# Performance work log

Measured on AMD Instinct MI355X. Metric: run time of the kernel, lower is better.

## Reference

```python
import jax, jax.numpy as jnp
import numpy as np

TEMPERATURE = 0.5
EPS = 1e-12  # torch F.normalize eps


def _l2_normalize(x, eps=EPS):
    n = jnp.linalg.norm(x, axis=1, keepdims=True)
    return x / jnp.maximum(n, eps)


def setup_inputs() -> dict:
    key = jax.random.key(0)
    k1, k2 = jax.random.split(key)
    B, D = 4096, 512
    return {
        "polyline_embs": jax.random.normal(k1, (B, D), dtype=jnp.float32),
        "c_embs": jax.random.normal(k2, (B, D), dtype=jnp.float32),
    }


def reference(polyline_embs, c_embs):
    b = polyline_embs.shape[0]
    # double-normalization in the original (F.normalize then cosine_similarity)
    # is idempotent on unit vectors, so sim = Z @ Z^T with Z unit-normalized.
    z = _l2_normalize(jnp.concatenate([polyline_embs, c_embs], axis=0))  # [2B, D]
    sim = z @ z.T  # [2B, 2B] cosine similarity
    # positives: diag offsets +B and -B
    idx = jnp.arange(b)
    sim_ij = sim[idx, idx + b]
    sim_ji = sim[idx + b, idx]
    positives = jnp.concatenate([sim_ij, sim_ji], axis=0)  # [2B]
    nominator = jnp.exp(positives / TEMPERATURE)
    mask = 1.0 - jnp.eye(2 * b, dtype=sim.dtype)
    denominator = jnp.sum(mask * jnp.exp(sim / TEMPERATURE), axis=1)  # [2B]
    all_losses = -jnp.log(nominator / denominator)
    return jnp.sum(all_losses) / (2 * b)
```

## Files before the change

kernel.cpp:

```cpp
#include <hip/hip_runtime.h>
#include <hip/hip_bf16.h>

#define B_ROWS 4096
#define D_DIM  512
#define N_ROWS 8192
#define BM 128
#define BN 128
#define BKB 128
#define NBLK (N_ROWS / BM)
#define NPAIR (NBLK * (NBLK + 1) / 2)

typedef float f32x4 __attribute__((ext_vector_type(4)));
typedef int   v4i   __attribute__((ext_vector_type(4)));
typedef int   v8i   __attribute__((ext_vector_type(8)));

__global__ __launch_bounds__(256) void prep_kernel(
    const float* __restrict__ poly, const float* __restrict__ cemb,
    unsigned char* __restrict__ Z, float* __restrict__ row_sum,
    float* __restrict__ pos, unsigned int* __restrict__ counter)
{
    const int wave = threadIdx.x >> 6;
    const int lane = threadIdx.x & 63;
    const int r = blockIdx.x * 4 + wave;

    const float4* prow = (const float4*)(poly + (size_t)r * D_DIM) + lane * 2;
    const float4* crow = (const float4*)(cemb + (size_t)r * D_DIM) + lane * 2;
    const float4 p0 = prow[0], p1 = prow[1];
    const float4 c0 = crow[0], c1 = crow[1];

    float ssp = p0.x*p0.x + p0.y*p0.y + p0.z*p0.z + p0.w*p0.w
              + p1.x*p1.x + p1.y*p1.y + p1.z*p1.z + p1.w*p1.w;
    float ssc = c0.x*c0.x + c0.y*c0.y + c0.z*c0.z + c0.w*c0.w
              + c1.x*c1.x + c1.y*c1.y + c1.z*c1.z + c1.w*c1.w;
    float dt  = p0.x*c0.x + p0.y*c0.y + p0.z*c0.z + p0.w*c0.w
              + p1.x*c1.x + p1.y*c1.y + p1.z*c1.z + p1.w*c1.w;

    #pragma unroll
    for (int m = 1; m < 64; m <<= 1) {
        ssp += __shfl_xor(ssp, m);
        ssc += __shfl_xor(ssc, m);
        dt  += __shfl_xor(dt,  m);
    }

    const float sp = 1.0f / fmaxf(sqrtf(ssp), 1e-12f);
    const float sc = 1.0f / fmaxf(sqrtf(ssc), 1e-12f);

    int2 zp, zc;
    zp.x = __builtin_amdgcn_cvt_pk_fp8_f32(p0.x*sp, p0.y*sp, 0, false)
         | (__builtin_amdgcn_cvt_pk_fp8_f32(p0.z*sp, p0.w*sp, 0, false) << 16);
    zp.y = __builtin_amdgcn_cvt_pk_fp8_f32(p1.x*sp, p1.y*sp, 0, false)
         | (__builtin_amdgcn_cvt_pk_fp8_f32(p1.z*sp, p1.w*sp, 0, false) << 16);
    zc.x = __builtin_amdgcn_cvt_pk_fp8_f32(c0.x*sc, c0.y*sc, 0, false)
         | (__builtin_amdgcn_cvt_pk_fp8_f32(c0.z*sc, c0.w*sc, 0, false) << 16);
    zc.y = __builtin_amdgcn_cvt_pk_fp8_f32(c1.x*sc, c1.y*sc, 0, false)
         | (__builtin_amdgcn_cvt_pk_fp8_f32(c1.z*sc, c1.w*sc, 0, false) << 16);

    *(int2*)(Z + (size_t)r * D_DIM + lane * 8)            = zp;
    *(int2*)(Z + (size_t)(r + B_ROWS) * D_DIM + lane * 8) = zc;

    if (lane == 0) {
        pos[r] = dt * sp * sc;
        row_sum[2 * r]     = 0.0f;
        row_sum[2 * r + 1] = 0.0f;
        if (r == 0) *counter = 0u;
    }
}

__global__ __launch_bounds__(512) void sim_kernel(
    const unsigned char* __restrict__ Z, float* __restrict__ row_sum,
    const float* __restrict__ pos, float* __restrict__ out,
    unsigned int* __restrict__ counter)
{
    __shared__ __align__(16) unsigned char As[BM * BKB];
    __shared__ __align__(16) unsigned char Bs[BN * BKB];
    __shared__ float rAcc[BM];
    __shared__ float cAcc[BN];
    __shared__ unsigned int lastFlag;

    const int t0 = blockIdx.x;
    int bi = (int)((129.0f - sqrtf(16641.0f - 8.0f * (float)t0)) * 0.5f);
    #define CFN(b) ((b) * (129 - (b)) / 2)
    while (CFN(bi + 1) <= t0) ++bi;
    while (CFN(bi) > t0) --bi;
    const int bj = bi + (t0 - CFN(bi));
    #undef CFN
    const bool diag = (bi == bj);

    const int ibase = bi * BM;
    const int jbase = bj * BN;
    const int tid   = threadIdx.x;

    const int srow = tid >> 3;
    const int gchk = (tid & 7) ^ (srow & 7);

    const int wave = tid >> 6;
    const int lane = tid & 63;
    const int wi = (wave >> 2) * 64;
    const int wj = (wave & 3) * 32;
    const int quad = lane >> 4;
    const int c    = lane & 15;

    f32x4 acc[4][2] = {};

    const int sg0 = (((quad << 1)    ) ^ (c & 7)) * 16;
    const int sg1 = (((quad << 1) | 1) ^ (c & 7)) * 16;

    #pragma unroll 1
    for (int k0 = 0; k0 < D_DIM; k0 += BKB) {
        #pragma unroll
        for (int it = 0; it < 2; ++it) {
            const int row = it * 64 + srow;
            const unsigned char* ga = Z + (size_t)(ibase + row) * D_DIM + k0 + gchk * 16;
            __builtin_amdgcn_global_load_lds(
                (const __attribute__((address_space(1))) void*)ga,
                (__attribute__((address_space(3))) void*)(As + it * 8192 + tid * 16),
                16, 0, 0);
        }
        if (!diag) {
            #pragma unroll
            for (int it = 0; it < 2; ++it) {
                const int row = it * 64 + srow;
                const unsigned char* gb = Z + (size_t)(jbase + row) * D_DIM + k0 + gchk * 16;
                __builtin_amdgcn_global_load_lds(
                    (const __attribute__((address_space(1))) void*)gb,
                    (__attribute__((address_space(3))) void*)(Bs + it * 8192 + tid * 16),
                    16, 0, 0);
            }
        }
        __syncthreads();

        const unsigned char* bb = diag ? As : Bs;

        v8i bfr[2];
        #pragma unroll
        for (int tj = 0; tj < 2; ++tj) {
            const unsigned char* base = bb + (wj + tj * 16 + c) * BKB;
            const v4i lo = *(const v4i*)(base + sg0);
            const v4i hi = *(const v4i*)(base + sg1);
            bfr[tj] = __builtin_shufflevector(lo, hi, 0, 1, 2, 3, 4, 5, 6, 7);
        }
        #pragma unroll
        for (int ti = 0; ti < 4; ++ti) {
            const unsigned char* base = As + (wi + ti * 16 + c) * BKB;
            const v4i lo = *(const v4i*)(base + sg0);
            const v4i hi = *(const v4i*)(base + sg1);
            const v8i afr = __builtin_shufflevector(lo, hi, 0, 1, 2, 3, 4, 5, 6, 7);
            #pragma unroll
            for (int tj = 0; tj < 2; ++tj)
                acc[ti][tj] = __builtin_amdgcn_mfma_scale_f32_16x16x128_f8f6f4(
                    afr, bfr[tj], acc[ti][tj],
                    0, 0,
                    0, 0x7f7f7f7f,
                    0, 0x7f7f7f7f);
        }
        __syncthreads();
    }

    if (tid < BM) { rAcc[tid] = 0.0f; cAcc[tid] = 0.0f; }
    __syncthreads();

    const float K2 = 2.885390081777927f;
    float col[2] = {0.0f, 0.0f};
    #pragma unroll
    for (int ti = 0; ti < 4; ++ti) {
        const int li = wi + ti * 16 + quad * 4;
        #pragma unroll
        for (int r = 0; r < 4; ++r) {
            const int gi = ibase + li + r;
            float v = 0.0f;
            #pragma unroll
            for (int tj = 0; tj < 2; ++tj) {
                const int gj = jbase + wj + tj * 16 + c;
                const float e = (gj > gi) ? exp2f(K2 * acc[ti][tj][r]) : 0.0f;
                v += e;
                col[tj] += e;
            }
            v += __shfl_xor(v, 1);
            v += __shfl_xor(v, 2);
            v += __shfl_xor(v, 4);
            v += __shfl_xor(v, 8);
            if (c == 0)
                atomicAdd(&rAcc[li + r], v);
        }
    }
    #pragma unroll
    for (int tj = 0; tj < 2; ++tj) {
        float w = col[tj];
        w += __shfl_xor(w, 16);
        w += __shfl_xor(w, 32);
        if (quad == 0)
            atomicAdd(&cAcc[wj + tj * 16 + c], w);
    }
    __syncthreads();

    if (tid < BM)
        atomicAdd(&row_sum[ibase + tid], rAcc[tid]);
    else if (tid < 2 * BM)
        atomicAdd(&row_sum[jbase + tid - BM], cAcc[tid - BM]);

    __syncthreads();
    if (tid == 0) {
        unsigned int old = __hip_atomic_fetch_add(
            counter, 1u, __ATOMIC_RELAXED, __HIP_MEMORY_SCOPE_AGENT);
        lastFlag = (old == NPAIR - 1) ? 1u : 0u;
    }
    __syncthreads();
    if (lastFlag) {
        float accL = 0.0f, accP = 0.0f;
        for (int i = tid; i < N_ROWS; i += 512) {
            const float rs = __hip_atomic_load(
                &row_sum[i], __ATOMIC_RELAXED, __HIP_MEMORY_SCOPE_AGENT);
            accL += __logf(rs);
        }
        for (int r = tid; r < B_ROWS; r += 512)
            accP += pos[r];
        #pragma unroll
        for (int m = 1; m < 64; m <<= 1) {
            accL += __shfl_xor(accL, m);
            accP += __shfl_xor(accP, m);
        }
        if (lane == 0) { rAcc[wave] = accL; cAcc[wave] = accP; }
        __syncthreads();
        if (tid == 0) {
            float L = 0.0f, P = 0.0f;
            #pragma unroll
            for (int w = 0; w < 8; ++w) { L += rAcc[w]; P += cAcc[w]; }
            out[0] = (L - 4.0f * P) / (float)N_ROWS;
        }
    }
}

extern "C" void kernel_launch(void* const* d_in, const int* in_sizes, int n_in,
                              void* d_out, int out_size, void* d_ws, size_t ws_size,
                              hipStream_t stream) {
    const float* poly = (const float*)d_in[0];
    const float* cemb = (const float*)d_in[1];

    unsigned char* Z       = (unsigned char*)d_ws;
    float*         row_sum = (float*)((char*)d_ws + (size_t)N_ROWS * D_DIM);
    float*         pos     = row_sum + N_ROWS;
    unsigned int*  counter = (unsigned int*)(pos + B_ROWS);
    float*         out     = (float*)d_out;

    prep_kernel<<<B_ROWS / 4, 256, 0, stream>>>(poly, cemb, Z, row_sum, pos, counter);
    sim_kernel<<<NPAIR, 512, 0, stream>>>(Z, row_sum, pos, out, counter);
}
```

Measured before the change: 121.0 us.

## Double-buffer LDS tiles and use DPP for intra-quad row reductions

Splits the LDS A/B tiles into two buffers so the async global-to-LDS load of the next K chunk is issued while MFMAs run on the current chunk, hiding load latency across the four K steps. It also swaps the first two shuffle-xor reduction steps for DPP quad-permute moves, which avoids LDS-based permutes. Doubling LDS to 64KB per block may lower occupancy. The loop keeps a single barrier per iteration, which raises the question of whether the next stage's writes can race with reads of the buffer still being consumed.

```diff
diff --git a/kernel.cpp b/kernel.cpp
--- a/kernel.cpp
+++ b/kernel.cpp
@@ -13,6 +13,15 @@
 typedef float f32x4 __attribute__((ext_vector_type(4)));
 typedef int   v4i   __attribute__((ext_vector_type(4)));
 typedef int   v8i   __attribute__((ext_vector_type(8)));
+
+__device__ __forceinline__ float dpp_xor1_add(float v) {
+    return v + __int_as_float(__builtin_amdgcn_mov_dpp(
+        __float_as_int(v), 0xB1, 0xf, 0xf, true));
+}
+__device__ __forceinline__ float dpp_xor2_add(float v) {
+    return v + __int_as_float(__builtin_amdgcn_mov_dpp(
+        __float_as_int(v), 0x4E, 0xf, 0xf, true));
+}
 
 __global__ __launch_bounds__(256) void prep_kernel(
     const float* __restrict__ poly, const float* __restrict__ cemb,
@@ -71,8 +80,8 @@
     const float* __restrict__ pos, float* __restrict__ out,
     unsigned int* __restrict__ counter)
 {
-    __shared__ __align__(16) unsigned char As[BM * BKB];
-    __shared__ __align__(16) unsigned char Bs[BN * BKB];
+    __shared__ __align__(16) unsigned char As[2][BM * BKB];
+    __shared__ __align__(16) unsigned char Bs[2][BN * BKB];
     __shared__ float rAcc[BM];
     __shared__ float cAcc[BN];
     __shared__ unsigned int lastFlag;
@@ -105,15 +114,14 @@
     const int sg0 = (((quad << 1)    ) ^ (c & 7)) * 16;
     const int sg1 = (((quad << 1) | 1) ^ (c & 7)) * 16;
 
-    #pragma unroll 1
-    for (int k0 = 0; k0 < D_DIM; k0 += BKB) {
+    auto stage = [&](int buf, int k0) {
         #pragma unroll
         for (int it = 0; it < 2; ++it) {
             const int row = it * 64 + srow;
             const unsigned char* ga = Z + (size_t)(ibase + row) * D_DIM + k0 + gchk * 16;
             __builtin_amdgcn_global_load_lds(
                 (const __attribute__((address_space(1))) void*)ga,
-                (__attribute__((address_space(3))) void*)(As + it * 8192 + tid * 16),
+                (__attribute__((address_space(3))) void*)(&As[buf][it * 8192 + tid * 16]),
                 16, 0, 0);
         }
         if (!diag) {
@@ -123,13 +131,21 @@
                 const unsigned char* gb = Z + (size_t)(jbase + row) * D_DIM + k0 + gchk * 16;
                 __builtin_amdgcn_global_load_lds(
                     (const __attribute__((address_space(1))) void*)gb,
-                    (__attribute__((address_space(3))) void*)(Bs + it * 8192 + tid * 16),
+                    (__attribute__((address_space(3))) void*)(&Bs[buf][it * 8192 + tid * 16]),
                     16, 0, 0);
             }
         }
-        __syncthreads();
-
-        const unsigned char* bb = diag ? As : Bs;
+    };
+
+    stage(0, 0);
+    __syncthreads();
+
+    #pragma unroll 1
+    for (int t = 0; t < 4; ++t) {
+        if (t < 3) stage((t + 1) & 1, (t + 1) * BKB);
+
+        const unsigned char* ab = As[t & 1];
+        const unsigned char* bb = diag ? ab : Bs[t & 1];
 
         v8i bfr[2];
         #pragma unroll
@@ -141,7 +157,7 @@
         }
         #pragma unroll
         for (int ti = 0; ti < 4; ++ti) {
-            const unsigned char* base = As + (wi + ti * 16 + c) * BKB;
+            const unsigned char* base = ab + (wi + ti * 16 + c) * BKB;
             const v4i lo = *(const v4i*)(base + sg0);
             const v4i hi = *(const v4i*)(base + sg1);
             const v8i afr = __builtin_shufflevector(lo, hi, 0, 1, 2, 3, 4, 5, 6, 7);
@@ -175,8 +191,8 @@
                 v += e;
                 col[tj] += e;
             }
-            v += __shfl_xor(v, 1);
-            v += __shfl_xor(v, 2);
+            v = dpp_xor1_add(v);
+            v = dpp_xor2_add(v);
             v += __shfl_xor(v, 4);
             v += __shfl_xor(v, 8);
             if (c == 0)
```

Result: no change. 122.3 us (+1.1%).

## Shrink sim block to two waves each computing a 64x128 tile

Applied to the files above, without the earlier changes.

The similarity kernel now runs 128 threads (2 waves) per 128x128 tile instead of 512 (8 waves). Each wave computes a 64x128 sub-tile with 32 accumulators, so every A fragment is reused across 8 B fragments and LDS fragment reads per MFMA drop. The first two steps of the row-sum reduction also use DPP moves instead of shuffles. The cost is much higher register pressure per wave, fewer waves per tile to hide load latency, and each thread issuing more global-to-LDS loads.

```diff
diff --git a/kernel.cpp b/kernel.cpp
--- a/kernel.cpp
+++ b/kernel.cpp
@@ -13,6 +13,15 @@
 typedef float f32x4 __attribute__((ext_vector_type(4)));
 typedef int   v4i   __attribute__((ext_vector_type(4)));
 typedef int   v8i   __attribute__((ext_vector_type(8)));
+
+__device__ __forceinline__ float dpp_xor1_add(float v) {
+    return v + __int_as_float(__builtin_amdgcn_mov_dpp(
+        __float_as_int(v), 0xB1, 0xf, 0xf, true));
+}
+__device__ __forceinline__ float dpp_xor2_add(float v) {
+    return v + __int_as_float(__builtin_amdgcn_mov_dpp(
+        __float_as_int(v), 0x4E, 0xf, 0xf, true));
+}
 
 __global__ __launch_bounds__(256) void prep_kernel(
     const float* __restrict__ poly, const float* __restrict__ cemb,
@@ -66,7 +75,7 @@
     }
 }
 
-__global__ __launch_bounds__(512) void sim_kernel(
+__global__ __launch_bounds__(128) void sim_kernel(
     const unsigned char* __restrict__ Z, float* __restrict__ row_sum,
     const float* __restrict__ pos, float* __restrict__ out,
     unsigned int* __restrict__ counter)
@@ -95,12 +104,12 @@
 
     const int wave = tid >> 6;
     const int lane = tid & 63;
-    const int wi = (wave >> 2) * 64;
-    const int wj = (wave & 3) * 32;
+    const int wi = wave * 64;
     const int quad = lane >> 4;
     const int c    = lane & 15;
 
-    f32x4 acc[4][2] = {};
+    f32x4 accA[4][4] = {};
+    f32x4 accB[4][4] = {};
 
     const int sg0 = (((quad << 1)    ) ^ (c & 7)) * 16;
     const int sg1 = (((quad << 1) | 1) ^ (c & 7)) * 16;
@@ -108,22 +117,22 @@
     #pragma unroll 1
     for (int k0 = 0; k0 < D_DIM; k0 += BKB) {
         #pragma unroll
-        for (int it = 0; it < 2; ++it) {
-            const int row = it * 64 + srow;
+        for (int it = 0; it < 8; ++it) {
+            const int row = it * 16 + srow;
             const unsigned char* ga = Z + (size_t)(ibase + row) * D_DIM + k0 + gchk * 16;
             __builtin_amdgcn_global_load_lds(
                 (const __attribute__((address_space(1))) void*)ga,
-                (__attribute__((address_space(3))) void*)(As + it * 8192 + tid * 16),
+                (__attribute__((address_space(3))) void*)(As + it * 2048 + tid * 16),
                 16, 0, 0);
         }
         if (!diag) {
             #pragma unroll
-            for (int it = 0; it < 2; ++it) {
-                const int row = it * 64 + srow;
+            for (int it = 0; it < 8; ++it) {
+                const int row = it * 16 + srow;
                 const unsigned char* gb = Z + (size_t)(jbase + row) * D_DIM + k0 + gchk * 16;
                 __builtin_amdgcn_global_load_lds(
                     (const __attribute__((address_space(1))) void*)gb,
-                    (__attribute__((address_space(3))) void*)(Bs + it * 8192 + tid * 16),
+                    (__attribute__((address_space(3))) void*)(Bs + it * 2048 + tid * 16),
                     16, 0, 0);
             }
         }
@@ -131,36 +140,41 @@
 
         const unsigned char* bb = diag ? As : Bs;
 
-        v8i bfr[2];
-        #pragma unroll
-        for (int tj = 0; tj < 2; ++tj) {
-            const unsigned char* base = bb + (wj + tj * 16 + c) * BKB;
-            const v4i lo = *(const v4i*)(base + sg0);
-            const v4i hi = *(const v4i*)(base + sg1);
-            bfr[tj] = __builtin_shufflevector(lo, hi, 0, 1, 2, 3, 4, 5, 6, 7);
-        }
+        v8i afr[4];
         #pragma unroll
         for (int ti = 0; ti < 4; ++ti) {
             const unsigned char* base = As + (wi + ti * 16 + c) * BKB;
             const v4i lo = *(const v4i*)(base + sg0);
             const v4i hi = *(const v4i*)(base + sg1);
-            const v8i afr = __builtin_shufflevector(lo, hi, 0, 1, 2, 3, 4, 5, 6, 7);
+            afr[ti] = __builtin_shufflevector(lo, hi, 0, 1, 2, 3, 4, 5, 6, 7);
+        }
+        #pragma unroll
+        for (int f = 0; f < 8; ++f) {
+            const unsigned char* base = bb + (f * 16 + c) * BKB;
+            const v4i lo = *(const v4i*)(base + sg0);
+            const v4i hi = *(const v4i*)(base + sg1);
+            const v8i bfr = __builtin_shufflevector(lo, hi, 0, 1, 2, 3, 4, 5, 6, 7);
             #pragma unroll
-            for (int tj = 0; tj < 2; ++tj)
-                acc[ti][tj] = __builtin_amdgcn_mfma_scale_f32_16x16x128_f8f6f4(
-                    afr, bfr[tj], acc[ti][tj],
-                    0, 0,
-                    0, 0x7f7f7f7f,
-                    0, 0x7f7f7f7f);
+            for (int ti = 0; ti < 4; ++ti) {
+                if (f < 4)
+                    accA[ti][f & 3] = __builtin_amdgcn_mfma_scale_f32_16x16x128_f8f6f4(
+                        afr[ti], bfr, accA[ti][f & 3], 0, 0,
+                        0, 0x7f7f7f7f, 0, 0x7f7f7f7f);
+                else
+                    accB[ti][f & 3] = __builtin_amdgcn_mfma_scale_f32_16x16x128_f8f6f4(
+                        afr[ti], bfr, accB[ti][f & 3], 0, 0,
+                        0, 0x7f7f7f7f, 0, 0x7f7f7f7f);
+            }
         }
         __syncthreads();
     }
 
-    if (tid < BM) { rAcc[tid] = 0.0f; cAcc[tid] = 0.0f; }
+    rAcc[tid] = 0.0f;
+    cAcc[tid] = 0.0f;
     __syncthreads();
 
     const float K2 = 2.885390081777927f;
-    float col[2] = {0.0f, 0.0f};
+    float col[8] = {0.0f, 0.0f, 0.0f, 0.0f, 0.0f, 0.0f, 0.0f, 0.0f};
     #pragma unroll
     for (int ti = 0; ti < 4; ++ti) {
         const int li = wi + ti * 16 + quad * 4;
@@ -169,14 +183,15 @@
             const int gi = ibase + li + r;
             float v = 0.0f;
             #pragma unroll
-            for (int tj = 0; tj < 2; ++tj) {
-                const int gj = jbase + wj + tj * 16 + c;
-                const float e = (gj > gi) ? exp2f(K2 * acc[ti][tj][r]) : 0.0f;
+            for (int f = 0; f < 8; ++f) {
+                const int gj = jbase + f * 16 + c;
+                const float s = (f < 4) ? accA[ti][f & 3][r] : accB[ti][f & 3][r];
+                const float e = (gj > gi) ? exp2f(K2 * s) : 0.0f;
                 v += e;
-                col[tj] += e;
+                col[f] += e;
             }
-            v += __shfl_xor(v, 1);
-            v += __shfl_xor(v, 2);
+            v = dpp_xor1_add(v);
+            v = dpp_xor2_add(v);
             v += __shfl_xor(v, 4);
             v += __shfl_xor(v, 8);
             if (c == 0)
@@ -184,19 +199,17 @@
         }
     }
     #pragma unroll
-    for (int tj = 0; tj < 2; ++tj) {
-        float w = col[tj];
+    for (int f = 0; f < 8; ++f) {
+        float w = col[f];
         w += __shfl_xor(w, 16);
         w += __shfl_xor(w, 32);
         if (quad == 0)
-            atomicAdd(&cAcc[wj + tj * 16 + c], w);
-    }
-    __syncthreads();
-
-    if (tid < BM)
-        atomicAdd(&row_sum[ibase + tid], rAcc[tid]);
-    else if (tid < 2 * BM)
-        atomicAdd(&row_sum[jbase + tid - BM], cAcc[tid - BM]);
+            atomicAdd(&cAcc[f * 16 + c], w);
+    }
+    __syncthreads();
+
+    atomicAdd(&row_sum[ibase + tid], rAcc[tid]);
+    atomicAdd(&row_sum[jbase + tid], cAcc[tid]);
 
     __syncthreads();
     if (tid == 0) {
@@ -207,12 +220,12 @@
     __syncthreads();
     if (lastFlag) {
         float accL = 0.0f, accP = 0.0f;
-        for (int i = tid; i < N_ROWS; i += 512) {
+        for (int i = tid; i < N_ROWS; i += 128) {
             const float rs = __hip_atomic_load(
                 &row_sum[i], __ATOMIC_RELAXED, __HIP_MEMORY_SCOPE_AGENT);
             accL += __logf(rs);
         }
-        for (int r = tid; r < B_ROWS; r += 512)
+        for (int r = tid; r < B_ROWS; r += 128)
             accP += pos[r];
         #pragma unroll
         for (int m = 1; m < 64; m <<= 1) {
@@ -222,10 +235,8 @@
         if (lane == 0) { rAcc[wave] = accL; cAcc[wave] = accP; }
         __syncthreads();
         if (tid == 0) {
-            float L = 0.0f, P = 0.0f;
-            #pragma unroll
-            for (int w = 0; w < 8; ++w) { L += rAcc[w]; P += cAcc[w]; }
-            out[0] = (L - 4.0f * P) / (float)N_ROWS;
+            out[0] = ((rAcc[0] + rAcc[1]) - 4.0f * (cAcc[0] + cAcc[1]))
+                     / (float)N_ROWS;
         }
     }
 }
@@ -243,5 +254,5 @@
     float*         out     = (float*)d_out;
 
     prep_kernel<<<B_ROWS / 4, 256, 0, stream>>>(poly, cemb, Z, row_sum, pos, counter);
-    sim_kernel<<<NPAIR, 512, 0, stream>>>(Z, row_sum, pos, out, counter);
-}
+    sim_kernel<<<NPAIR, 128, 0, stream>>>(Z, row_sum, pos, out, counter);
+}
```

Result: slower. 154.4 us (+27.6%).
